# Performance work log

Hardware: AMD Instinct MI355X
Metric: run time of the kernel (lower is better)

## Reference

```python
import jax, jax.numpy as jnp
import numpy as np

N_HEAD = 16    # config.n_head
T_STEPS = 3    # config.T: PC energy-minimization steps
LR = 0.01      # config.local_learning_rate


def _causal_attention(x, Wq, Wk, Wv):
    # x: [B, S, E] latent activity; generative model f(x) = causal MHA(x)
    B, S, E = x.shape
    D = E // N_HEAD
    def split(h):  # [B,S,E] -> [B,H,S,D]
        return h.reshape(B, S, N_HEAD, D).transpose(0, 2, 1, 3)
    q = split(x @ Wq.T)
    k = split(x @ Wk.T)
    v = split(x @ Wv.T)
    scores = jnp.einsum('bhqd,bhkd->bhqk', q, k) / jnp.sqrt(jnp.asarray(D, x.dtype))
    mask = jnp.tril(jnp.ones((S, S), dtype=bool))
    scores = jnp.where(mask, scores, jnp.asarray(-1e30, x.dtype))
    att = jax.nn.softmax(scores, axis=-1)
    out = jnp.einsum('bhqk,bhkd->bhqd', att, v)
    return out.transpose(0, 2, 1, 3).reshape(B, S, E)


def _pc_infer(target, f):
    # PCLayer: T steps of gradient descent on E(x) = 0.5 * ||target - f(x)||^2
    # x_init = 'zeros'; returns the inferred latent x (PCLayer.get_x).
    x = jnp.zeros_like(target)
    energy = lambda z: 0.5 * jnp.sum((target - f(z)) ** 2)
    g = jax.grad(energy)
    for _ in range(T_STEPS):  # fixed small T: unrolled
        x = x - LR * g(x)
    return x


def setup_inputs() -> dict:
    key = jax.random.key(0)
    ks = jax.random.split(key, 5)
    B, S, E = 2, 1024, 1024
    fc1_x = jax.random.normal(ks[0], (B, S, E), dtype=jnp.float32)
    init = lambda k: 0.02 * jax.random.normal(k, (E, E), dtype=jnp.float32)
    return {
        'fc1_x': fc1_x,
        'Wq': init(ks[1]),
        'Wk': init(ks[2]),
        'Wv': init(ks[3]),
        'Wo': init(ks[4]),
    }


def reference(fc1_x, Wq, Wk, Wv, Wo):
    # Stage 1 (pc_output): infer pre-output latent att_score s.t. output-proj
    # Wo @ att_score ~ fc1_x  (generative model f1(x) = x @ Wo^T, bias=False).
    att_score = _pc_infer(fc1_x, lambda z: z @ Wo.T)
    # Stage 2 (pc_qkv): infer latent x_qkv s.t. causal MHA(x_qkv) ~ att_score.
    x_qkv = _pc_infer(att_score, lambda z: _causal_attention(z, Wq, Wk, Wv))
    return x_qkv
```

## Files before the change

kernel.cpp:

```cpp
#include <hip/hip_runtime.h>
#include <hip/hip_bf16.h>
#include <math.h>

#define S_LEN 1024
#define E_DIM 1024
#define NH 16
#define HD 64
#define M_ROWS 2048
#define BH_CNT 32

static constexpr float LR_C = 0.01f;
static constexpr float SC_C = 0.125f;
static constexpr float C2_C = 0.125f * 1.44269504f;

typedef unsigned short ushort_t;
typedef __attribute__((ext_vector_type(8))) __bf16 bf16x8;
typedef __attribute__((ext_vector_type(4))) float f32x4;

static __device__ inline ushort_t f2bu(float f) {
  __hip_bfloat16 h = __float2bfloat16(f);
  return *(ushort_t*)&h;
}
static __device__ inline bf16x8 ldg8(const ushort_t* p) { return *(const bf16x8*)p; }

static __device__ inline void async_cp16(const ushort_t* g, __bf16* lds_wave_base) {
  __builtin_amdgcn_global_load_lds((const __attribute__((address_space(1))) void*)g,
                                   (__attribute__((address_space(3))) void*)lds_wave_base,
                                   16, 0, 0);
}

static __device__ inline void stage_tile(const ushort_t* src, size_t src_stride,
                                         ushort_t* lds, int lane, int wave) {
  int rl = lane >> 3;
  int c = ((lane & 7) - rl) & 7;
  #pragma unroll
  for (int t = 0; t < 2; t++) {
    int s = wave * 2 + t;
    async_cp16(src + (size_t)(s * 8 + rl) * src_stride + c * 8,
               (__bf16*)(lds + s * 512));
  }
}
static __device__ inline const bf16x8* tile_at(const ushort_t* lds, int r, int cchunk) {
  return (const bf16x8*)(lds + r * 64 + (((cchunk + r) & 7) * 8));
}

__global__ __launch_bounds__(256) void prep_w(const float* __restrict__ W,
                                              ushort_t* __restrict__ Wb,
                                              ushort_t* __restrict__ WTb) {
  __shared__ float ts[64][65];
  int bx = blockIdx.x * 64, by = blockIdx.y * 64;
  int t = threadIdx.x;
  int rr = t >> 6, cc = t & 63;
  #pragma unroll
  for (int p = 0; p < 16; p++) {
    int r = p * 4 + rr;
    float v = W[(size_t)(by + r) * E_DIM + bx + cc];
    ts[r][cc] = v;
    Wb[(size_t)(by + r) * E_DIM + bx + cc] = f2bu(v);
  }
  __syncthreads();
  #pragma unroll
  for (int p = 0; p < 16; p++) {
    int r = p * 4 + rr;
    WTb[(size_t)(bx + r) * E_DIM + by + cc] = f2bu(ts[cc][r]);
  }
}

__global__ __launch_bounds__(256) void k_cast(const float* __restrict__ in,
                                              ushort_t* __restrict__ out, int n4) {
  int i = blockIdx.x * 256 + threadIdx.x;
  if (i < n4) {
    float4 v = ((const float4*)in)[i];
    ushort_t p[4] = {f2bu(v.x), f2bu(v.y), f2bu(v.z), f2bu(v.w)};
    *(uint2*)(out + (size_t)i * 4) = *(uint2*)p;
  }
}

__global__ __launch_bounds__(256) void k_formN(const float* __restrict__ Mf,
                                               const float* __restrict__ M2f,
                                               ushort_t* __restrict__ Nb) {
  int idx = blockIdx.x * 256 + threadIdx.x;
  int i = idx >> 10, j = idx & 1023;
  float v = -3.f * LR_C * LR_C * Mf[idx] + LR_C * LR_C * LR_C * M2f[idx];
  if (i == j) v += 3.f * LR_C;
  Nb[idx] = f2bu(v);
}

__global__ __launch_bounds__(256) void k_scan1(const float* __restrict__ Xs,
                                               float* __restrict__ Sf,
                                               float* __restrict__ tot) {
  int e = blockIdx.x * 256 + threadIdx.x;
  int b = blockIdx.y;
  int z = blockIdx.z;
  float acc = 0.f;
  for (int i = z * 64 + 63; i >= z * 64; i--) {
    size_t idx = ((size_t)b * S_LEN + i) * E_DIM + e;
    acc = fmaf(Xs[idx], 1.0f / (float)(i + 1), acc);
    Sf[idx] = acc;
  }
  tot[((size_t)b * 16 + z) * E_DIM + e] = acc;
}

__global__ __launch_bounds__(256) void k_scan2(const float* __restrict__ Sf,
                                               const float* __restrict__ tot,
                                               ushort_t* __restrict__ Sb) {
  int e = blockIdx.x * 256 + threadIdx.x;
  int b = blockIdx.y;
  int z = blockIdx.z;
  float off = 0.f;
  for (int c = z + 1; c < 16; c++) off += tot[((size_t)b * 16 + c) * E_DIM + e];
  for (int i = z * 64; i < z * 64 + 64; i++) {
    size_t idx = ((size_t)b * S_LEN + i) * E_DIM + e;
    Sb[idx] = f2bu(Sf[idx] + off);
  }
}

template <int MODE, int NSEG>
__global__ __launch_bounds__(256) void gemm_mf(
    const ushort_t* __restrict__ A0, const ushort_t* __restrict__ A1, const ushort_t* __restrict__ A2,
    const ushort_t* __restrict__ B0, const ushort_t* __restrict__ B1, const ushort_t* __restrict__ B2,
    float* __restrict__ Cf,
    ushort_t* __restrict__ Cb0,
    float alpha) {
  const int K = 1024;
  __shared__ __bf16 As0[64][32];
  __shared__ __bf16 As1[64][32];
  __shared__ __bf16 Bs0[64][32];
  __shared__ __bf16 Bs1[64][32];
  int tid = threadIdx.x;
  int m0 = blockIdx.y * 64, n0 = blockIdx.x * 64;

  int lane = tid & 63, wave = tid >> 6;
  int wrow = wave >> 1, wcol = wave & 1;
  int fr = lane & 15, q = lane >> 4;

  int srow = wave * 16 + (lane >> 2);
  int scg = ((lane & 3) + (srow >> 1)) & 3;
  int scol = scg * 8;
  __bf16* ldsA0 = &As0[wave * 16][0];
  __bf16* ldsA1 = &As1[wave * 16][0];
  __bf16* ldsB0 = &Bs0[wave * 16][0];
  __bf16* ldsB1 = &Bs1[wave * 16][0];

  int rA0 = wrow * 32 + fr, rA1r = rA0 + 16;
  int rB0 = wcol * 32 + fr, rB1r = rB0 + 16;
  int cA0 = ((q - (rA0 >> 1)) & 3) * 8;
  int cA1 = ((q - (rA1r >> 1)) & 3) * 8;
  int cB0 = ((q - (rB0 >> 1)) & 3) * 8;
  int cB1 = ((q - (rB1r >> 1)) & 3) * 8;
  const bf16x8* pa0h0 = (const bf16x8*)&As0[rA0][cA0];
  const bf16x8* pa0h1 = (const bf16x8*)&As1[rA0][cA0];
  const bf16x8* pa1h0 = (const bf16x8*)&As0[rA1r][cA1];
  const bf16x8* pa1h1 = (const bf16x8*)&As1[rA1r][cA1];
  const bf16x8* pb0h0 = (const bf16x8*)&Bs0[rB0][cB0];
  const bf16x8* pb0h1 = (const bf16x8*)&Bs1[rB0][cB0];
  const bf16x8* pb1h0 = (const bf16x8*)&Bs0[rB1r][cB1];
  const bf16x8* pb1h1 = (const bf16x8*)&Bs1[rB1r][cB1];

  f32x4 acc[2][2] = {};

  #pragma unroll 1
  for (int seg = 0; seg < NSEG; seg++) {
    const ushort_t* Aseg = (seg == 0) ? A0 : (seg == 1) ? A1 : A2;
    const ushort_t* Bseg = (seg == 0) ? B0 : (seg == 1) ? B1 : B2;
    const ushort_t* ga = Aseg + (size_t)(m0 + srow) * K + scol;
    const ushort_t* gb = Bseg + (size_t)(n0 + srow) * K + scol;
    #pragma unroll 1
    for (int k0 = 0; k0 < K; k0 += 64) {
      __syncthreads();
      async_cp16(ga + k0, ldsA0);
      async_cp16(ga + k0 + 32, ldsA1);
      async_cp16(gb + k0, ldsB0);
      async_cp16(gb + k0 + 32, ldsB1);
      __syncthreads();
      bf16x8 a00 = *pa0h0, a01 = *pa0h1, a10 = *pa1h0, a11 = *pa1h1;
      bf16x8 b00 = *pb0h0, b01 = *pb0h1, b10 = *pb1h0, b11 = *pb1h1;
      acc[0][0] = __builtin_amdgcn_mfma_f32_16x16x32_bf16(a00, b00, acc[0][0], 0, 0, 0);
      acc[0][1] = __builtin_amdgcn_mfma_f32_16x16x32_bf16(a00, b10, acc[0][1], 0, 0, 0);
      acc[1][0] = __builtin_amdgcn_mfma_f32_16x16x32_bf16(a10, b00, acc[1][0], 0, 0, 0);
      acc[1][1] = __builtin_amdgcn_mfma_f32_16x16x32_bf16(a10, b10, acc[1][1], 0, 0, 0);
      acc[0][0] = __builtin_amdgcn_mfma_f32_16x16x32_bf16(a01, b01, acc[0][0], 0, 0, 0);
      acc[0][1] = __builtin_amdgcn_mfma_f32_16x16x32_bf16(a01, b11, acc[0][1], 0, 0, 0);
      acc[1][0] = __builtin_amdgcn_mfma_f32_16x16x32_bf16(a11, b01, acc[1][0], 0, 0, 0);
      acc[1][1] = __builtin_amdgcn_mfma_f32_16x16x32_bf16(a11, b11, acc[1][1], 0, 0, 0);
    }
  }

  #pragma unroll
  for (int mi = 0; mi < 2; mi++)
    #pragma unroll
    for (int ni = 0; ni < 2; ni++) {
      int col = n0 + wcol * 32 + ni * 16 + fr;
      int row0 = m0 + wrow * 32 + mi * 16 + q * 4;
      #pragma unroll
      for (int r = 0; r < 4; r++) {
        size_t idx = (size_t)(row0 + r) * E_DIM + col;
        float v = acc[mi][ni][r];
        if (MODE == 3) {
          Cf[idx] = v;
        } else if (MODE == 4) {
          Cf[idx] = v;
          Cb0[idx] = f2bu(v);
        } else if (MODE == 6) {
          float nv = alpha * v;
          Cf[idx] = nv;
          Cb0[idx] = f2bu(nv);
        } else {
          Cb0[idx] = f2bu(v);
        }
      }
    }
}

__global__ __launch_bounds__(256) void gemm_qkv(
    const ushort_t* __restrict__ A,
    const ushort_t* __restrict__ B0, const ushort_t* __restrict__ B1, const ushort_t* __restrict__ B2,
    ushort_t* __restrict__ Cb0, ushort_t* __restrict__ Cb1, ushort_t* __restrict__ Cb2,
    ushort_t* __restrict__ Ct0, ushort_t* __restrict__ Ct1, ushort_t* __restrict__ Ct2) {
  const int K = 1024;
  __shared__ __bf16 As[2][64][32];
  __shared__ __bf16 Bs[3][2][64][32];
  int tid = threadIdx.x;
  int m0 = blockIdx.y * 64, n0 = blockIdx.x * 64;

  int lane = tid & 63, wave = tid >> 6;
  int wrow = wave >> 1, wcol = wave & 1;
  int fr = lane & 15, q = lane >> 4;

  int srow = wave * 16 + (lane >> 2);
  int scg = ((lane & 3) + (srow >> 1)) & 3;
  int scol = scg * 8;
  __bf16* ldsA0 = &As[0][wave * 16][0];
  __bf16* ldsA1 = &As[1][wave * 16][0];
  __bf16* ldsB00 = &Bs[0][0][wave * 16][0];
  __bf16* ldsB01 = &Bs[0][1][wave * 16][0];
  __bf16* ldsB10 = &Bs[1][0][wave * 16][0];
  __bf16* ldsB11 = &Bs[1][1][wave * 16][0];
  __bf16* ldsB20 = &Bs[2][0][wave * 16][0];
  __bf16* ldsB21 = &Bs[2][1][wave * 16][0];

  int rA0 = wrow * 32 + fr, rA1r = rA0 + 16;
  int rB0 = wcol * 32 + fr, rB1r = rB0 + 16;
  int cA0 = ((q - (rA0 >> 1)) & 3) * 8;
  int cA1 = ((q - (rA1r >> 1)) & 3) * 8;
  int cB0 = ((q - (rB0 >> 1)) & 3) * 8;
  int cB1 = ((q - (rB1r >> 1)) & 3) * 8;
  const bf16x8* pa0h0 = (const bf16x8*)&As[0][rA0][cA0];
  const bf16x8* pa0h1 = (const bf16x8*)&As[1][rA0][cA0];
  const bf16x8* pa1h0 = (const bf16x8*)&As[0][rA1r][cA1];
  const bf16x8* pa1h1 = (const bf16x8*)&As[1][rA1r][cA1];

  f32x4 acc[3][2][2] = {};

  const ushort_t* ga = A + (size_t)(m0 + srow) * K + scol;
  const ushort_t* gb0 = B0 + (size_t)(n0 + srow) * K + scol;
  const ushort_t* gb1 = B1 + (size_t)(n0 + srow) * K + scol;
  const ushort_t* gb2 = B2 + (size_t)(n0 + srow) * K + scol;

  #pragma unroll 1
  for (int k0 = 0; k0 < K; k0 += 64) {
    __syncthreads();
    async_cp16(ga + k0, ldsA0);
    async_cp16(ga + k0 + 32, ldsA1);
    async_cp16(gb0 + k0, ldsB00);
    async_cp16(gb0 + k0 + 32, ldsB01);
    async_cp16(gb1 + k0, ldsB10);
    async_cp16(gb1 + k0 + 32, ldsB11);
    async_cp16(gb2 + k0, ldsB20);
    async_cp16(gb2 + k0 + 32, ldsB21);
    __syncthreads();
    bf16x8 a00 = *pa0h0, a01 = *pa0h1, a10 = *pa1h0, a11 = *pa1h1;
    #pragma unroll
    for (int z = 0; z < 3; z++) {
      bf16x8 b00 = *(const bf16x8*)&Bs[z][0][rB0][cB0];
      bf16x8 b01 = *(const bf16x8*)&Bs[z][1][rB0][cB0];
      bf16x8 b10 = *(const bf16x8*)&Bs[z][0][rB1r][cB1];
      bf16x8 b11 = *(const bf16x8*)&Bs[z][1][rB1r][cB1];
      acc[z][0][0] = __builtin_amdgcn_mfma_f32_16x16x32_bf16(a00, b00, acc[z][0][0], 0, 0, 0);
      acc[z][0][1] = __builtin_amdgcn_mfma_f32_16x16x32_bf16(a00, b10, acc[z][0][1], 0, 0, 0);
      acc[z][1][0] = __builtin_amdgcn_mfma_f32_16x16x32_bf16(a10, b00, acc[z][1][0], 0, 0, 0);
      acc[z][1][1] = __builtin_amdgcn_mfma_f32_16x16x32_bf16(a10, b10, acc[z][1][1], 0, 0, 0);
      acc[z][0][0] = __builtin_amdgcn_mfma_f32_16x16x32_bf16(a01, b01, acc[z][0][0], 0, 0, 0);
      acc[z][0][1] = __builtin_amdgcn_mfma_f32_16x16x32_bf16(a01, b11, acc[z][0][1], 0, 0, 0);
      acc[z][1][0] = __builtin_amdgcn_mfma_f32_16x16x32_bf16(a11, b01, acc[z][1][0], 0, 0, 0);
      acc[z][1][1] = __builtin_amdgcn_mfma_f32_16x16x32_bf16(a11, b11, acc[z][1][1], 0, 0, 0);
    }
  }

  #pragma unroll
  for (int z = 0; z < 3; z++) {
    ushort_t* Cbz = (z == 0) ? Cb0 : (z == 1) ? Cb1 : Cb2;
    ushort_t* Ctz = (z == 0) ? Ct0 : (z == 1) ? Ct1 : Ct2;
    float tsc = (z == 2) ? 1.0f : SC_C;
    #pragma unroll
    for (int mi = 0; mi < 2; mi++)
      #pragma unroll
      for (int ni = 0; ni < 2; ni++) {
        int col = n0 + wcol * 32 + ni * 16 + fr;
        int row0 = m0 + wrow * 32 + mi * 16 + q * 4;
        ushort_t pk[4];
        #pragma unroll
        for (int r = 0; r < 4; r++) {
          size_t idx = (size_t)(row0 + r) * E_DIM + col;
          float v = acc[z][mi][ni][r];
          Cbz[idx] = f2bu(v);
          pk[r] = f2bu(v * tsc);
        }
        int hh = col >> 6, dd = col & 63;
        int bb = row0 >> 10, ss = row0 & 1023;
        *(uint2*)(Ctz + ((size_t)((bb * NH + hh) * HD + dd)) * S_LEN + ss) = *(uint2*)pk;
      }
  }
}

__global__ __launch_bounds__(256) void gemm_acc(
    const ushort_t* __restrict__ A0, const ushort_t* __restrict__ A1, const ushort_t* __restrict__ A2,
    const ushort_t* __restrict__ B0, const ushort_t* __restrict__ B1, const ushort_t* __restrict__ B2,
    float* __restrict__ Cf, ushort_t* __restrict__ Cb, float alpha) {
  const int K = 1024;
  __shared__ __bf16 As[3][2][64][32];
  __shared__ __bf16 Bs[3][2][64][32];
  int tid = threadIdx.x;
  int m0 = blockIdx.y * 64, n0 = blockIdx.x * 64;

  int lane = tid & 63, wave = tid >> 6;
  int wrow = wave >> 1, wcol = wave & 1;
  int fr = lane & 15, q = lane >> 4;

  int srow = wave * 16 + (lane >> 2);
  int scg = ((lane & 3) + (srow >> 1)) & 3;
  int scol = scg * 8;

  int rA0 = wrow * 32 + fr, rA1r = rA0 + 16;
  int rB0 = wcol * 32 + fr, rB1r = rB0 + 16;
  int cA0 = ((q - (rA0 >> 1)) & 3) * 8;
  int cA1 = ((q - (rA1r >> 1)) & 3) * 8;
  int cB0 = ((q - (rB0 >> 1)) & 3) * 8;
  int cB1 = ((q - (rB1r >> 1)) & 3) * 8;

  f32x4 acc[3][2][2] = {};

  const ushort_t* ga0 = A0 + (size_t)(m0 + srow) * K + scol;
  const ushort_t* ga1 = A1 + (size_t)(m0 + srow) * K + scol;
  const ushort_t* ga2 = A2 + (size_t)(m0 + srow) * K + scol;
  const ushort_t* gb0 = B0 + (size_t)(n0 + srow) * K + scol;
  const ushort_t* gb1 = B1 + (size_t)(n0 + srow) * K + scol;
  const ushort_t* gb2 = B2 + (size_t)(n0 + srow) * K + scol;

  #pragma unroll 1
  for (int k0 = 0; k0 < K; k0 += 64) {
    __syncthreads();
    async_cp16(ga0 + k0,      &As[0][0][wave * 16][0]);
    async_cp16(ga0 + k0 + 32, &As[0][1][wave * 16][0]);
    async_cp16(ga1 + k0,      &As[1][0][wave * 16][0]);
    async_cp16(ga1 + k0 + 32, &As[1][1][wave * 16][0]);
    async_cp16(ga2 + k0,      &As[2][0][wave * 16][0]);
    async_cp16(ga2 + k0 + 32, &As[2][1][wave * 16][0]);
    async_cp16(gb0 + k0,      &Bs[0][0][wave * 16][0]);
    async_cp16(gb0 + k0 + 32, &Bs[0][1][wave * 16][0]);
    async_cp16(gb1 + k0,      &Bs[1][0][wave * 16][0]);
    async_cp16(gb1 + k0 + 32, &Bs[1][1][wave * 16][0]);
    async_cp16(gb2 + k0,      &Bs[2][0][wave * 16][0]);
    async_cp16(gb2 + k0 + 32, &Bs[2][1][wave * 16][0]);
    __syncthreads();
    #pragma unroll
    for (int z = 0; z < 3; z++) {
      bf16x8 a00 = *(const bf16x8*)&As[z][0][rA0][cA0];
      bf16x8 a01 = *(const bf16x8*)&As[z][1][rA0][cA0];
      bf16x8 a10 = *(const bf16x8*)&As[z][0][rA1r][cA1];
      bf16x8 a11 = *(const bf16x8*)&As[z][1][rA1r][cA1];
      bf16x8 b00 = *(const bf16x8*)&Bs[z][0][rB0][cB0];
      bf16x8 b01 = *(const bf16x8*)&Bs[z][1][rB0][cB0];
      bf16x8 b10 = *(const bf16x8*)&Bs[z][0][rB1r][cB1];
      bf16x8 b11 = *(const bf16x8*)&Bs[z][1][rB1r][cB1];
      acc[z][0][0] = __builtin_amdgcn_mfma_f32_16x16x32_bf16(a00, b00, acc[z][0][0], 0, 0, 0);
      acc[z][0][1] = __builtin_amdgcn_mfma_f32_16x16x32_bf16(a00, b10, acc[z][0][1], 0, 0, 0);
      acc[z][1][0] = __builtin_amdgcn_mfma_f32_16x16x32_bf16(a10, b00, acc[z][1][0], 0, 0, 0);
      acc[z][1][1] = __builtin_amdgcn_mfma_f32_16x16x32_bf16(a10, b10, acc[z][1][1], 0, 0, 0);
      acc[z][0][0] = __builtin_amdgcn_mfma_f32_16x16x32_bf16(a01, b01, acc[z][0][0], 0, 0, 0);
      acc[z][0][1] = __builtin_amdgcn_mfma_f32_16x16x32_bf16(a01, b11, acc[z][0][1], 0, 0, 0);
      acc[z][1][0] = __builtin_amdgcn_mfma_f32_16x16x32_bf16(a11, b01, acc[z][1][0], 0, 0, 0);
      acc[z][1][1] = __builtin_amdgcn_mfma_f32_16x16x32_bf16(a11, b11, acc[z][1][1], 0, 0, 0);
    }
  }

  #pragma unroll
  for (int mi = 0; mi < 2; mi++)
    #pragma unroll
    for (int ni = 0; ni < 2; ni++) {
      int col = n0 + wcol * 32 + ni * 16 + fr;
      int row0 = m0 + wrow * 32 + mi * 16 + q * 4;
      #pragma unroll
      for (int r = 0; r < 4; r++) {
        size_t idx = (size_t)(row0 + r) * E_DIM + col;
        float v = (acc[0][mi][ni][r] + acc[1][mi][ni][r]) + acc[2][mi][ni][r];
        float nv = Cf[idx] + alpha * v;
        Cf[idx] = nv;
        Cb[idx] = f2bu(nv);
      }
    }
}


__global__ __launch_bounds__(256) void fwd_fused(const ushort_t* __restrict__ Qg,
                                                 const ushort_t* __restrict__ Kg,
                                                 const ushort_t* __restrict__ Vt,
                                                 const float* __restrict__ Xs,
                                                 float* __restrict__ mbuf,
                                                 ushort_t* __restrict__ Gb,
                                                 ushort_t* __restrict__ Gt,
                                                 float* __restrict__ Dv) {
  int bh = blockIdx.x, y = blockIdx.y;
  int it = (y < 8) ? (15 - y) : (y - 8);
  int b = bh >> 4, h = bh & 15;
  int tid = threadIdx.x, lane = tid & 63, wv = tid >> 6;
  int fr = lane & 15, q = lane >> 4;
  int i0 = it * 64, band = wv * 16;
  __shared__ ushort_t Ksb[2][4096];
  __shared__ ushort_t Vsb[2][4096];
  __shared__ ushort_t Ps[64][72];

  const ushort_t* Kbase = Kg + (size_t)(b * S_LEN) * E_DIM + h * HD;
  const ushort_t* Vbase = Vt + (size_t)(bh * HD) * S_LEN;

  const ushort_t* Qrow = Qg + (size_t)(b * S_LEN + i0 + band + fr) * E_DIM + h * HD;
  bf16x8 aq0 = ldg8(Qrow + q * 8);
  bf16x8 aq1 = ldg8(Qrow + 32 + q * 8);

  float m[4], l[4];
  #pragma unroll
  for (int r = 0; r < 4; r++) { m[r] = -1e30f; l[r] = 0.f; }
  f32x4 oacc[4] = {};

  stage_tile(Kbase, E_DIM, Ksb[0], lane, wv);
  stage_tile(Vbase, S_LEN, Vsb[0], lane, wv);

  #pragma unroll 1
  for (int jt = 0; jt <= it; jt++) {
    int j0 = jt * 64;
    int cur = jt & 1;
    __syncthreads();
    if (jt < it) {
      int j0n = j0 + 64;
      stage_tile(Kbase + (size_t)j0n * E_DIM, E_DIM, Ksb[cur ^ 1], lane, wv);
      stage_tile(Vbase + j0n, S_LEN, Vsb[cur ^ 1], lane, wv);
    }
    const ushort_t* Ks = Ksb[cur];
    const ushort_t* Vs = Vsb[cur];
    f32x4 sA[4];
    #pragma unroll
    for (int nc = 0; nc < 4; nc++) {
      bf16x8 bk0 = *tile_at(Ks, nc * 16 + fr, q);
      bf16x8 bk1 = *tile_at(Ks, nc * 16 + fr, q + 4);
      f32x4 z = {};
      z = __builtin_amdgcn_mfma_f32_16x16x32_bf16(aq0, bk0, z, 0, 0, 0);
      sA[nc] = __builtin_amdgcn_mfma_f32_16x16x32_bf16(aq1, bk1, z, 0, 0, 0);
    }
    float sv[4][4];
    if (jt == it) {
      #pragma unroll
      for (int nc = 0; nc < 4; nc++)
        #pragma unroll
        for (int r = 0; r < 4; r++) {
          int row = i0 + band + q * 4 + r;
          int col = j0 + nc * 16 + fr;
          sv[nc][r] = (col <= row) ? sA[nc][r] * C2_C : -1e30f;
        }
    } else {
      #pragma unroll
      for (int nc = 0; nc < 4; nc++)
        #pragma unroll
        for (int r = 0; r < 4; r++)
          sv[nc][r] = sA[nc][r] * C2_C;
    }
    #pragma unroll
    for (int r = 0; r < 4; r++) {
      float mx = fmaxf(fmaxf(sv[0][r], sv[1][r]), fmaxf(sv[2][r], sv[3][r]));
      #pragma unroll
      for (int off = 1; off < 16; off <<= 1) mx = fmaxf(mx, __shfl_xor(mx, off, 64));
      float mn = fmaxf(m[r], mx);
      float alpha = exp2f(m[r] - mn);
      float ps = 0.f;
      #pragma unroll
      for (int nc = 0; nc < 4; nc++) {
        float p = exp2f(sv[nc][r] - mn);
        Ps[band + q * 4 + r][nc * 16 + fr] = f2bu(p);
        ps += p;
      }
      l[r] = l[r] * alpha + ps;
      m[r] = mn;
      #pragma unroll
      for (int nc = 0; nc < 4; nc++) oacc[nc][r] *= alpha;
    }
    bf16x8 ap0 = *(const bf16x8*)&Ps[band + fr][q * 8];
    bf16x8 ap1 = *(const bf16x8*)&Ps[band + fr][32 + q * 8];
    #pragma unroll
    for (int nc = 0; nc < 4; nc++) {
      bf16x8 bv0 = *tile_at(Vs, nc * 16 + fr, q);
      bf16x8 bv1 = *tile_at(Vs, nc * 16 + fr, q + 4);
      oacc[nc] = __builtin_amdgcn_mfma_f32_16x16x32_bf16(ap0, bv0, oacc[nc], 0, 0, 0);
      oacc[nc] = __builtin_amdgcn_mfma_f32_16x16x32_bf16(ap1, bv1, oacc[nc], 0, 0, 0);
    }
  }
  #pragma unroll
  for (int r = 0; r < 4; r++) {
    #pragma unroll
    for (int off = 1; off < 16; off <<= 1) l[r] += __shfl_xor(l[r], off, 64);
  }
  float linv[4];
  #pragma unroll
  for (int r = 0; r < 4; r++) linv[r] = 1.0f / l[r];
  float dpart[4] = {};
  #pragma unroll
  for (int nc = 0; nc < 4; nc++) {
    ushort_t pg[4];
    #pragma unroll
    for (int r = 0; r < 4; r++) {
      int row = i0 + band + q * 4 + r;
      size_t gi = (size_t)(b * S_LEN + row) * E_DIM + h * HD + nc * 16 + fr;
      float o = oacc[nc][r] * linv[r];
      float g = o - Xs[gi];
      ushort_t bu = f2bu(g);
      Gb[gi] = bu;
      pg[r] = bu;
      dpart[r] += g * o;
    }
    int d = nc * 16 + fr;
    int s0 = i0 + band + q * 4;
    *(uint2*)(Gt + ((size_t)bh * HD + d) * S_LEN + s0) = *(uint2*)pg;
  }
  #pragma unroll
  for (int r = 0; r < 4; r++) {
    #pragma unroll
    for (int off = 1; off < 16; off <<= 1) dpart[r] += __shfl_xor(dpart[r], off, 64);
  }
  if (fr == 0) {
    #pragma unroll
    for (int r = 0; r < 4; r++) {
      size_t sid = (size_t)bh * S_LEN + i0 + band + q * 4 + r;
      mbuf[sid] = m[r] + log2f(l[r]);
      Dv[sid] = dpart[r];
    }
  }
}

__global__ __launch_bounds__(256) void bwd_fused(const ushort_t* __restrict__ Qg,
                                                 const ushort_t* __restrict__ Kg,
                                                 const ushort_t* __restrict__ Vg,
                                                 const ushort_t* __restrict__ Gg,
                                                 const ushort_t* __restrict__ Qt,
                                                 const ushort_t* __restrict__ Kt,
                                                 const ushort_t* __restrict__ Gt,
                                                 const float* __restrict__ mbuf,
                                                 const float* __restrict__ Dv,
                                                 ushort_t* __restrict__ GQ,
                                                 ushort_t* __restrict__ GK,
                                                 ushort_t* __restrict__ GV) {
  int bh = blockIdx.x, y = blockIdx.y;
  int b = bh >> 4, h = bh & 15;
  int tid = threadIdx.x, lane = tid & 63, wv = tid >> 6;
  int fr = lane & 15, q = lane >> 4;
  int band = wv * 16;
  __shared__ ushort_t tA[4][4096];
  __shared__ ushort_t tP[2][64][72];

  {
    ushort_t* Ks = tA[0];
    ushort_t* Vs = tA[1];
    ushort_t* Ts = tA[2];
    ushort_t (*dSs)[72] = tP[0];
    int it = y, i0 = it * 64;

    const ushort_t* KbaseA = Kg + (size_t)(b * S_LEN) * E_DIM + h * HD;
    const ushort_t* VbaseA = Vg + (size_t)(b * S_LEN) * E_DIM + h * HD;
    const ushort_t* TbaseA = Kt + (size_t)(bh * HD) * S_LEN;

    const ushort_t* Qrow = Qg + (size_t)(b * S_LEN + i0 + band + fr) * E_DIM + h * HD;
    const ushort_t* Grow = Gg + (size_t)(b * S_LEN + i0 + band + fr) * E_DIM + h * HD;
    bf16x8 aq0 = ldg8(Qrow + q * 8), aq1 = ldg8(Qrow + 32 + q * 8);
    bf16x8 ag0 = ldg8(Grow + q * 8), ag1 = ldg8(Grow + 32 + q * 8);

    float mrow[4], Dr[4];
    #pragma unroll
    for (int r = 0; r < 4; r++) {
      size_t sid = (size_t)bh * S_LEN + i0 + band + q * 4 + r;
      mrow[r] = mbuf[sid]; Dr[r] = Dv[sid];
    }
    f32x4 dqacc[4] = {};

    #pragma unroll 1
    for (int jt = 0; jt <= it; jt++) {
      int j0 = jt * 64;
      __syncthreads();
      stage_tile(KbaseA + (size_t)j0 * E_DIM, E_DIM, Ks, lane, wv);
      stage_tile(VbaseA + (size_t)j0 * E_DIM, E_DIM, Vs, lane, wv);
      stage_tile(TbaseA + j0, S_LEN, Ts, lane, wv);
      __syncthreads();
      f32x4 sA[4], dpA[4];
      #pragma unroll
      for (int nc = 0; nc < 4; nc++) {
        bf16x8 bk0 = *tile_at(Ks, nc * 16 + fr, q);
        bf16x8 bk1 = *tile_at(Ks, nc * 16 + fr, q + 4);
        bf16x8 bv0 = *tile_at(Vs, nc * 16 + fr, q);
        bf16x8 bv1 = *tile_at(Vs, nc * 16 + fr, q + 4);
        f32x4 z = {};
        z = __builtin_amdgcn_mfma_f32_16x16x32_bf16(aq0, bk0, z, 0, 0, 0);
        sA[nc] = __builtin_amdgcn_mfma_f32_16x16x32_bf16(aq1, bk1, z, 0, 0, 0);
        f32x4 z2 = {};
        z2 = __builtin_amdgcn_mfma_f32_16x16x32_bf16(ag0, bv0, z2, 0, 0, 0);
        dpA[nc] = __builtin_amdgcn_mfma_f32_16x16x32_bf16(ag1, bv1, z2, 0, 0, 0);
      }
      if (jt == it) {
        #pragma unroll
        for (int nc = 0; nc < 4; nc++)
          #pragma unroll
          for (int r = 0; r < 4; r++) {
            int row = i0 + band + q * 4 + r;
            int col = j0 + nc * 16 + fr;
            float ds = 0.f;
            if (col <= row) {
              float P = exp2f(fmaf(sA[nc][r], C2_C, -mrow[r]));
              ds = P * (dpA[nc][r] - Dr[r]);
            }
            dSs[band + q * 4 + r][nc * 16 + fr] = f2bu(ds);
          }
      } else {
        #pragma unroll
        for (int nc = 0; nc < 4; nc++)
          #pragma unroll
          for (int r = 0; r < 4; r++) {
            float P = exp2f(fmaf(sA[nc][r], C2_C, -mrow[r]));
            float ds = P * (dpA[nc][r] - Dr[r]);
            dSs[band + q * 4 + r][nc * 16 + fr] = f2bu(ds);
          }
      }
      bf16x8 ad0 = *(const bf16x8*)&dSs[band + fr][q * 8];
      bf16x8 ad1 = *(const bf16x8*)&dSs[band + fr][32 + q * 8];
      #pragma unroll
      for (int nc = 0; nc < 4; nc++) {
        bf16x8 bt0 = *tile_at(Ts, nc * 16 + fr, q);
        bf16x8 bt1 = *tile_at(Ts, nc * 16 + fr, q + 4);
        dqacc[nc] = __builtin_amdgcn_mfma_f32_16x16x32_bf16(ad0, bt0, dqacc[nc], 0, 0, 0);
        dqacc[nc] = __builtin_amdgcn_mfma_f32_16x16x32_bf16(ad1, bt1, dqacc[nc], 0, 0, 0);
      }
    }
    #pragma unroll
    for (int nc = 0; nc < 4; nc++)
      #pragma unroll
      for (int r = 0; r < 4; r++) {
        int row = i0 + band + q * 4 + r;
        size_t gi = (size_t)(b * S_LEN + row) * E_DIM + h * HD + nc * 16 + fr;
        GQ[gi] = f2bu(dqacc[nc][r]);
      }
  }

  {
    ushort_t* Qs  = tA[0];
    ushort_t* Gs  = tA[1];
    ushort_t* Qts = tA[2];
    ushort_t* Gts = tA[3];
    ushort_t (*PT)[72]  = tP[0];
    ushort_t (*dST)[72] = tP[1];
    int jt = y, j0 = jt * 64;

    const ushort_t* QbaseB = Qg + (size_t)(b * S_LEN) * E_DIM + h * HD;
    const ushort_t* GbaseB = Gg + (size_t)(b * S_LEN) * E_DIM + h * HD;
    const ushort_t* QtbaseB = Qt + (size_t)(bh * HD) * S_LEN;
    const ushort_t* GtbaseB = Gt + (size_t)(bh * HD) * S_LEN;

    const ushort_t* Krow = Kg + (size_t)(b * S_LEN + j0 + band + fr) * E_DIM + h * HD;
    const ushort_t* Vrow = Vg + (size_t)(b * S_LEN + j0 + band + fr) * E_DIM + h * HD;
    bf16x8 ak0 = ldg8(Krow + q * 8), ak1 = ldg8(Krow + 32 + q * 8);
    bf16x8 av0 = ldg8(Vrow + q * 8), av1 = ldg8(Vrow + 32 + q * 8);

    f32x4 dkacc[4] = {}, dvacc[4] = {};

    #pragma unroll 1
    for (int i_t = jt; i_t < 16; i_t++) {
      int i0 = i_t * 64;
      __syncthreads();
      stage_tile(QbaseB + (size_t)i0 * E_DIM, E_DIM, Qs, lane, wv);
      stage_tile(GbaseB + (size_t)i0 * E_DIM, E_DIM, Gs, lane, wv);
      stage_tile(QtbaseB + i0, S_LEN, Qts, lane, wv);
      stage_tile(GtbaseB + i0, S_LEN, Gts, lane, wv);
      __syncthreads();
      float mc[4], Dc[4];
      #pragma unroll
      for (int nc = 0; nc < 4; nc++) {
        size_t sid = (size_t)bh * S_LEN + i0 + nc * 16 + fr;
        mc[nc] = mbuf[sid]; Dc[nc] = Dv[sid];
      }
      f32x4 stA[4], dptA[4];
      #pragma unroll
      for (int nc = 0; nc < 4; nc++) {
        bf16x8 bq0 = *tile_at(Qs, nc * 16 + fr, q);
        bf16x8 bq1 = *tile_at(Qs, nc * 16 + fr, q + 4);
        bf16x8 bg0 = *tile_at(Gs, nc * 16 + fr, q);
        bf16x8 bg1 = *tile_at(Gs, nc * 16 + fr, q + 4);
        f32x4 z = {};
        z = __builtin_amdgcn_mfma_f32_16x16x32_bf16(ak0, bq0, z, 0, 0, 0);
        stA[nc] = __builtin_amdgcn_mfma_f32_16x16x32_bf16(ak1, bq1, z, 0, 0, 0);
        f32x4 z2 = {};
        z2 = __builtin_amdgcn_mfma_f32_16x16x32_bf16(av0, bg0, z2, 0, 0, 0);
        dptA[nc] = __builtin_amdgcn_mfma_f32_16x16x32_bf16(av1, bg1, z2, 0, 0, 0);
      }
      if (i_t == jt) {
        #pragma unroll
        for (int nc = 0; nc < 4; nc++)
          #pragma unroll
          for (int r = 0; r < 4; r++) {
            int jrow = j0 + band + q * 4 + r;
            int icol = i0 + nc * 16 + fr;
            float P = 0.f, ds = 0.f;
            if (icol >= jrow) {
              P = exp2f(fmaf(stA[nc][r], C2_C, -mc[nc]));
              ds = P * (dptA[nc][r] - Dc[nc]);
            }
            PT[band + q * 4 + r][nc * 16 + fr] = f2bu(P);
            dST[band + q * 4 + r][nc * 16 + fr] = f2bu(ds);
          }
      } else {
        #pragma unroll
        for (int nc = 0; nc < 4; nc++)
          #pragma unroll
          for (int r = 0; r < 4; r++) {
            float P = exp2f(fmaf(stA[nc][r], C2_C, -mc[nc]));
            float ds = P * (dptA[nc][r] - Dc[nc]);
            PT[band + q * 4 + r][nc * 16 + fr] = f2bu(P);
            dST[band + q * 4 + r][nc * 16 + fr] = f2bu(ds);
          }
      }
      bf16x8 ap0 = *(const bf16x8*)&PT[band + fr][q * 8];
      bf16x8 ap1 = *(const bf16x8*)&PT[band + fr][32 + q * 8];
      bf16x8 ad0 = *(const bf16x8*)&dST[band + fr][q * 8];
      bf16x8 ad1 = *(const bf16x8*)&dST[band + fr][32 + q * 8];
      #pragma unroll
      for (int nc = 0; nc < 4; nc++) {
        bf16x8 bg0 = *tile_at(Gts, nc * 16 + fr, q);
        bf16x8 bg1 = *tile_at(Gts, nc * 16 + fr, q + 4);
        bf16x8 bq0 = *tile_at(Qts, nc * 16 + fr, q);
        bf16x8 bq1 = *tile_at(Qts, nc * 16 + fr, q + 4);
        dvacc[nc] = __builtin_amdgcn_mfma_f32_16x16x32_bf16(ap0, bg0, dvacc[nc], 0, 0, 0);
        dvacc[nc] = __builtin_amdgcn_mfma_f32_16x16x32_bf16(ap1, bg1, dvacc[nc], 0, 0, 0);
        dkacc[nc] = __builtin_amdgcn_mfma_f32_16x16x32_bf16(ad0, bq0, dkacc[nc], 0, 0, 0);
        dkacc[nc] = __builtin_amdgcn_mfma_f32_16x16x32_bf16(ad1, bq1, dkacc[nc], 0, 0, 0);
      }
    }
    #pragma unroll
    for (int nc = 0; nc < 4; nc++)
      #pragma unroll
      for (int r = 0; r < 4; r++) {
        int jrow = j0 + band + q * 4 + r;
        size_t gi = (size_t)(b * S_LEN + jrow) * E_DIM + h * HD + nc * 16 + fr;
        GK[gi] = f2bu(dkacc[nc][r]);
        GV[gi] = f2bu(dvacc[nc][r]);
      }
  }
}

extern "C" void kernel_launch(void* const* d_in, const int* in_sizes, int n_in,
                              void* d_out, int out_size, void* d_ws, size_t ws_size,
                              hipStream_t stream) {
  const float* T1 = (const float*)d_in[0];
  const float* Wq = (const float*)d_in[1];
  const float* Wk = (const float*)d_in[2];
  const float* Wv = (const float*)d_in[3];
  const float* Wo = (const float*)d_in[4];

  const size_t M2 = 2097152;
  const size_t M1 = 1048576;
  float* w = (float*)d_ws;
  float* Xs = w;
  float* mS = Xs + M2;
  float* DvS = mS + 65536;
  ushort_t* u = (ushort_t*)(DvS + 65536);
  ushort_t* W0 = u;          ushort_t* W1 = W0 + M1;  ushort_t* W2 = W1 + M1;
  ushort_t* W3 = W2 + M1;    ushort_t* W4 = W3 + M1;  ushort_t* W5 = W4 + M1;
  ushort_t* Qb = W5 + M1;    ushort_t* Kb = Qb + M2;  ushort_t* Vb = Kb + M2;
  ushort_t* Qt = Vb + M2;    ushort_t* Kt = Qt + M2;  ushort_t* Vt = Kt + M2;
  ushort_t* Gt = Vt + M2;
  ushort_t* Gb = Gt + M2;
  ushort_t* GQb = Gb + M2;   ushort_t* GKb = GQb + M2; ushort_t* GVb = GKb + M2;
  ushort_t* X2b = GVb + M2;
  float* X2 = (float*)d_out;

  float* Mf  = (float*)Qb;
  float* M2f = (float*)Kb;
  ushort_t* Mb  = Gt;
  ushort_t* Nb  = Vb;
  ushort_t* AtB = Qt;
  ushort_t* T1b = Kt;

  float* Sf  = (float*)GQb;
  float* tot = mS;
  ushort_t* Sb = GVb;

  dim3 pgrid(16, 16);
  dim3 sgrid(16, 16);
  dim3 ggrid(16, 32);
  dim3 agrid(BH_CNT, 16);

  k_cast<<<(M2 / 4 + 255) / 256, 256, 0, stream>>>(T1, T1b, (int)(M2 / 4));
  prep_w<<<pgrid, 256, 0, stream>>>(Wo, W0, W1);
  gemm_mf<4, 1><<<sgrid, 256, 0, stream>>>(W1, nullptr, nullptr, W1, nullptr, nullptr,
                                           Mf, Mb, 0.f);
  gemm_mf<3, 1><<<sgrid, 256, 0, stream>>>(Mb, nullptr, nullptr, Mb, nullptr, nullptr,
                                           M2f, nullptr, 0.f);
  k_formN<<<(M1 + 255) / 256, 256, 0, stream>>>(Mf, M2f, Nb);
  gemm_mf<5, 1><<<sgrid, 256, 0, stream>>>(Nb, nullptr, nullptr, W0, nullptr, nullptr,
                                           nullptr, AtB, 0.f);
  prep_w<<<pgrid, 256, 0, stream>>>(Wq, W0, W3);
  prep_w<<<pgrid, 256, 0, stream>>>(Wk, W1, W4);
  prep_w<<<pgrid, 256, 0, stream>>>(Wv, W2, W5);
  gemm_mf<3, 1><<<ggrid, 256, 0, stream>>>(T1b, nullptr, nullptr, AtB, nullptr, nullptr,
                                           Xs, nullptr, 0.f);

  k_scan1<<<dim3(E_DIM / 256, 2, 16), 256, 0, stream>>>(Xs, Sf, tot);
  k_scan2<<<dim3(E_DIM / 256, 2, 16), 256, 0, stream>>>(Sf, tot, Sb);
  gemm_mf<6, 1><<<ggrid, 256, 0, stream>>>(Sb, nullptr, nullptr, W5, nullptr, nullptr,
                                           X2, X2b, LR_C);

  for (int t = 1; t < 3; t++) {
    gemm_qkv<<<ggrid, 256, 0, stream>>>(X2b, W0, W1, W2,
                                        Qb, Kb, Vb, Qt, Kt, Vt);
    fwd_fused<<<agrid, 256, 0, stream>>>(Qb, Kb, Vt, Xs, mS, Gb, Gt, DvS);
    bwd_fused<<<agrid, 256, 0, stream>>>(Qb, Kb, Vb, Gb, Qt, Kt, Gt, mS, DvS,
                                         GQb, GKb, GVb);
    gemm_acc<<<ggrid, 256, 0, stream>>>(GQb, GKb, GVb, W3, W4, W5,
                                        X2, X2b, -LR_C);
  }
}
```

Baseline: 407.7 us.

## Double-buffer GEMM LDS tiles, merge weight prep, fuse formN into GEMM epilogue

Adds double-buffered LDS staging to gemm_mf and gemm_qkv so the async copies for the next K-tile are issued while MFMAs consume the current one, dropping one barrier per iteration. The four weight-prep launches become one launch with a z grid dimension. The N-matrix formation kernel is folded into a new epilogue mode of the M^2 GEMM, which removes a kernel and an fp32 intermediate. Shared memory per block doubles, which may reduce occupancy. The per-iteration barrier now sits before the prefetch issue, so correctness depends on how async_cp16 completion is waited on.

```diff
diff --git a/kernel.cpp b/kernel.cpp
--- a/kernel.cpp
+++ b/kernel.cpp
@@ -44,10 +44,18 @@
   return (const bf16x8*)(lds + r * 64 + (((cchunk + r) & 7) * 8));
 }
 
-__global__ __launch_bounds__(256) void prep_w(const float* __restrict__ W,
-                                              ushort_t* __restrict__ Wb,
-                                              ushort_t* __restrict__ WTb) {
+__global__ __launch_bounds__(256) void prep_w4(
+    const float* __restrict__ Wo, const float* __restrict__ Wq,
+    const float* __restrict__ Wk, const float* __restrict__ Wv,
+    ushort_t* __restrict__ o0, ushort_t* __restrict__ t0,
+    ushort_t* __restrict__ o1, ushort_t* __restrict__ t1,
+    ushort_t* __restrict__ o2, ushort_t* __restrict__ t2,
+    ushort_t* __restrict__ o3, ushort_t* __restrict__ t3) {
   __shared__ float ts[64][65];
+  int z = blockIdx.z;
+  const float* W = (z == 0) ? Wo : (z == 1) ? Wq : (z == 2) ? Wk : Wv;
+  ushort_t* Wb  = (z == 0) ? o0 : (z == 1) ? o1 : (z == 2) ? o2 : o3;
+  ushort_t* WTb = (z == 0) ? t0 : (z == 1) ? t1 : (z == 2) ? t2 : t3;
   int bx = blockIdx.x * 64, by = blockIdx.y * 64;
   int t = threadIdx.x;
   int rr = t >> 6, cc = t & 63;
@@ -74,16 +82,6 @@
     ushort_t p[4] = {f2bu(v.x), f2bu(v.y), f2bu(v.z), f2bu(v.w)};
     *(uint2*)(out + (size_t)i * 4) = *(uint2*)p;
   }
-}
-
-__global__ __launch_bounds__(256) void k_formN(const float* __restrict__ Mf,
-                                               const float* __restrict__ M2f,
-                                               ushort_t* __restrict__ Nb) {
-  int idx = blockIdx.x * 256 + threadIdx.x;
-  int i = idx >> 10, j = idx & 1023;
-  float v = -3.f * LR_C * LR_C * Mf[idx] + LR_C * LR_C * LR_C * M2f[idx];
-  if (i == j) v += 3.f * LR_C;
-  Nb[idx] = f2bu(v);
 }
 
 __global__ __launch_bounds__(256) void k_scan1(const float* __restrict__ Xs,
@@ -115,18 +113,13 @@
   }
 }
 
-template <int MODE, int NSEG>
+template <int MODE>
 __global__ __launch_bounds__(256) void gemm_mf(
-    const ushort_t* __restrict__ A0, const ushort_t* __restrict__ A1, const ushort_t* __restrict__ A2,
-    const ushort_t* __restrict__ B0, const ushort_t* __restrict__ B1, const ushort_t* __restrict__ B2,
-    float* __restrict__ Cf,
-    ushort_t* __restrict__ Cb0,
-    float alpha) {
+    const ushort_t* __restrict__ A, const ushort_t* __restrict__ B,
+    float* __restrict__ Cf, ushort_t* __restrict__ Cb0, float alpha) {
   const int K = 1024;
-  __shared__ __bf16 As0[64][32];
-  __shared__ __bf16 As1[64][32];
-  __shared__ __bf16 Bs0[64][32];
-  __shared__ __bf16 Bs1[64][32];
+  __shared__ __bf16 As[2][2][64][32];
+  __shared__ __bf16 Bs[2][2][64][32];
   int tid = threadIdx.x;
   int m0 = blockIdx.y * 64, n0 = blockIdx.x * 64;
 
@@ -137,10 +130,6 @@
   int srow = wave * 16 + (lane >> 2);
   int scg = ((lane & 3) + (srow >> 1)) & 3;
   int scol = scg * 8;
-  __bf16* ldsA0 = &As0[wave * 16][0];
-  __bf16* ldsA1 = &As1[wave * 16][0];
-  __bf16* ldsB0 = &Bs0[wave * 16][0];
-  __bf16* ldsB1 = &Bs1[wave * 16][0];
 
   int rA0 = wrow * 32 + fr, rA1r = rA0 + 16;
   int rB0 = wcol * 32 + fr, rB1r = rB0 + 16;
@@ -148,42 +137,44 @@
   int cA1 = ((q - (rA1r >> 1)) & 3) * 8;
   int cB0 = ((q - (rB0 >> 1)) & 3) * 8;
   int cB1 = ((q - (rB1r >> 1)) & 3) * 8;
-  const bf16x8* pa0h0 = (const bf16x8*)&As0[rA0][cA0];
-  const bf16x8* pa0h1 = (const bf16x8*)&As1[rA0][cA0];
-  const bf16x8* pa1h0 = (const bf16x8*)&As0[rA1r][cA1];
-  const bf16x8* pa1h1 = (const bf16x8*)&As1[rA1r][cA1];
-  const bf16x8* pb0h0 = (const bf16x8*)&Bs0[rB0][cB0];
-  const bf16x8* pb0h1 = (const bf16x8*)&Bs1[rB0][cB0];
-  const bf16x8* pb1h0 = (const bf16x8*)&Bs0[rB1r][cB1];
-  const bf16x8* pb1h1 = (const bf16x8*)&Bs1[rB1r][cB1];
+
+  const ushort_t* ga = A + (size_t)(m0 + srow) * K + scol;
+  const ushort_t* gb = B + (size_t)(n0 + srow) * K + scol;
 
   f32x4 acc[2][2] = {};
 
+  async_cp16(ga,      &As[0][0][wave * 16][0]);
+  async_cp16(ga + 32, &As[0][1][wave * 16][0]);
+  async_cp16(gb,      &Bs[0][0][wave * 16][0]);
+  async_cp16(gb + 32, &Bs[0][1][wave * 16][0]);
+
   #pragma unroll 1
-  for (int seg = 0; seg < NSEG; seg++) {
-    const ushort_t* Aseg = (seg == 0) ? A0 : (seg == 1) ? A1 : A2;
-    const ushort_t* Bseg = (seg == 0) ? B0 : (seg == 1) ? B1 : B2;
-    const ushort_t* ga = Aseg + (size_t)(m0 + srow) * K + scol;
-    const ushort_t* gb = Bseg + (size_t)(n0 + srow) * K + scol;
-    #pragma unroll 1
-    for (int k0 = 0; k0 < K; k0 += 64) {
-      __syncthreads();
-      async_cp16(ga + k0, ldsA0);
-      async_cp16(ga + k0 + 32, ldsA1);
-      async_cp16(gb + k0, ldsB0);
-      async_cp16(gb + k0 + 32, ldsB1);
-      __syncthreads();
-      bf16x8 a00 = *pa0h0, a01 = *pa0h1, a10 = *pa1h0, a11 = *pa1h1;
-      bf16x8 b00 = *pb0h0, b01 = *pb0h1, b10 = *pb1h0, b11 = *pb1h1;
-      acc[0][0] = __builtin_amdgcn_mfma_f32_16x16x32_bf16(a00, b00, acc[0][0], 0, 0, 0);
-      acc[0][1] = __builtin_amdgcn_mfma_f32_16x16x32_bf16(a00, b10, acc[0][1], 0, 0, 0);
-      acc[1][0] = __builtin_amdgcn_mfma_f32_16x16x32_bf16(a10, b00, acc[1][0], 0, 0, 0);
-      acc[1][1] = __builtin_amdgcn_mfma_f32_16x16x32_bf16(a10, b10, acc[1][1], 0, 0, 0);
-      acc[0][0] = __builtin_amdgcn_mfma_f32_16x16x32_bf16(a01, b01, acc[0][0], 0, 0, 0);
-      acc[0][1] = __builtin_amdgcn_mfma_f32_16x16x32_bf16(a01, b11, acc[0][1], 0, 0, 0);
-      acc[1][0] = __builtin_amdgcn_mfma_f32_16x16x32_bf16(a11, b01, acc[1][0], 0, 0, 0);
-      acc[1][1] = __builtin_amdgcn_mfma_f32_16x16x32_bf16(a11, b11, acc[1][1], 0, 0, 0);
-    }
+  for (int k0 = 0; k0 < K; k0 += 64) {
+    int cur = (k0 >> 6) & 1;
+    __syncthreads();
+    if (k0 + 64 < K) {
+      int nxt = cur ^ 1;
+      async_cp16(ga + k0 + 64, &As[nxt][0][wave * 16][0]);
+      async_cp16(ga + k0 + 96, &As[nxt][1][wave * 16][0]);
+      async_cp16(gb + k0 + 64, &Bs[nxt][0][wave * 16][0]);
+      async_cp16(gb + k0 + 96, &Bs[nxt][1][wave * 16][0]);
+    }
+    bf16x8 a00 = *(const bf16x8*)&As[cur][0][rA0][cA0];
+    bf16x8 a01 = *(const bf16x8*)&As[cur][1][rA0][cA0];
+    bf16x8 a10 = *(const bf16x8*)&As[cur][0][rA1r][cA1];
+    bf16x8 a11 = *(const bf16x8*)&As[cur][1][rA1r][cA1];
+    bf16x8 b00 = *(const bf16x8*)&Bs[cur][0][rB0][cB0];
+    bf16x8 b01 = *(const bf16x8*)&Bs[cur][1][rB0][cB0];
+    bf16x8 b10 = *(const bf16x8*)&Bs[cur][0][rB1r][cB1];
+    bf16x8 b11 = *(const bf16x8*)&Bs[cur][1][rB1r][cB1];
+    acc[0][0] = __builtin_amdgcn_mfma_f32_16x16x32_bf16(a00, b00, acc[0][0], 0, 0, 0);
+    acc[0][1] = __builtin_amdgcn_mfma_f32_16x16x32_bf16(a00, b10, acc[0][1], 0, 0, 0);
+    acc[1][0] = __builtin_amdgcn_mfma_f32_16x16x32_bf16(a10, b00, acc[1][0], 0, 0, 0);
+    acc[1][1] = __builtin_amdgcn_mfma_f32_16x16x32_bf16(a10, b10, acc[1][1], 0, 0, 0);
+    acc[0][0] = __builtin_amdgcn_mfma_f32_16x16x32_bf16(a01, b01, acc[0][0], 0, 0, 0);
+    acc[0][1] = __builtin_amdgcn_mfma_f32_16x16x32_bf16(a01, b11, acc[0][1], 0, 0, 0);
+    acc[1][0] = __builtin_amdgcn_mfma_f32_16x16x32_bf16(a11, b01, acc[1][0], 0, 0, 0);
+    acc[1][1] = __builtin_amdgcn_mfma_f32_16x16x32_bf16(a11, b11, acc[1][1], 0, 0, 0);
   }
 
   #pragma unroll
@@ -205,6 +196,10 @@
           float nv = alpha * v;
           Cf[idx] = nv;
           Cb0[idx] = f2bu(nv);
+        } else if (MODE == 7) {
+          float nv = -3.f * LR_C * LR_C * Cf[idx] + LR_C * LR_C * LR_C * v;
+          if (row0 + r == col) nv += 3.f * LR_C;
+          Cb0[idx] = f2bu(nv);
         } else {
           Cb0[idx] = f2bu(v);
         }
@@ -218,8 +213,8 @@
     ushort_t* __restrict__ Cb0, ushort_t* __restrict__ Cb1, ushort_t* __restrict__ Cb2,
     ushort_t* __restrict__ Ct0, ushort_t* __restrict__ Ct1, ushort_t* __restrict__ Ct2) {
   const int K = 1024;
-  __shared__ __bf16 As[2][64][32];
-  __shared__ __bf16 Bs[3][2][64][32];
+  __shared__ __bf16 As[2][2][64][32];
+  __shared__ __bf16 Bs[2][3][2][64][32];
   int tid = threadIdx.x;
   int m0 = blockIdx.y * 64, n0 = blockIdx.x * 64;
 
@@ -230,14 +225,6 @@
   int srow = wave * 16 + (lane >> 2);
   int scg = ((lane & 3) + (srow >> 1)) & 3;
   int scol = scg * 8;
-  __bf16* ldsA0 = &As[0][wave * 16][0];
-  __bf16* ldsA1 = &As[1][wave * 16][0];
-  __bf16* ldsB00 = &Bs[0][0][wave * 16][0];
-  __bf16* ldsB01 = &Bs[0][1][wave * 16][0];
-  __bf16* ldsB10 = &Bs[1][0][wave * 16][0];
-  __bf16* ldsB11 = &Bs[1][1][wave * 16][0];
-  __bf16* ldsB20 = &Bs[2][0][wave * 16][0];
-  __bf16* ldsB21 = &Bs[2][1][wave * 16][0];
 
   int rA0 = wrow * 32 + fr, rA1r = rA0 + 16;
   int rB0 = wcol * 32 + fr, rB1r = rB0 + 16;
@@ -245,37 +232,48 @@
   int cA1 = ((q - (rA1r >> 1)) & 3) * 8;
   int cB0 = ((q - (rB0 >> 1)) & 3) * 8;
   int cB1 = ((q - (rB1r >> 1)) & 3) * 8;
-  const bf16x8* pa0h0 = (const bf16x8*)&As[0][rA0][cA0];
-  const bf16x8* pa0h1 = (const bf16x8*)&As[1][rA0][cA0];
-  const bf16x8* pa1h0 = (const bf16x8*)&As[0][rA1r][cA1];
-  const bf16x8* pa1h1 = (const bf16x8*)&As[1][rA1r][cA1];
-
-  f32x4 acc[3][2][2] = {};
 
   const ushort_t* ga = A + (size_t)(m0 + srow) * K + scol;
   const ushort_t* gb0 = B0 + (size_t)(n0 + srow) * K + scol;
   const ushort_t* gb1 = B1 + (size_t)(n0 + srow) * K + scol;
   const ushort_t* gb2 = B2 + (size_t)(n0 + srow) * K + scol;
 
+  f32x4 acc[3][2][2] = {};
+
+  async_cp16(ga,       &As[0][0][wave * 16][0]);
+  async_cp16(ga + 32,  &As[0][1][wave * 16][0]);
+  async_cp16(gb0,      &Bs[0][0][0][wave * 16][0]);
+  async_cp16(gb0 + 32, &Bs[0][0][1][wave * 16][0]);
+  async_cp16(gb1,      &Bs[0][1][0][wave * 16][0]);
+  async_cp16(gb1 + 32, &Bs[0][1][1][wave * 16][0]);
+  async_cp16(gb2,      &Bs[0][2][0][wave * 16][0]);
+  async_cp16(gb2 + 32, &Bs[0][2][1][wave * 16][0]);
+
   #pragma unroll 1
   for (int k0 = 0; k0 < K; k0 += 64) {
+    int cur = (k0 >> 6) & 1;
     __syncthreads();
-    async_cp16(ga + k0, ldsA0);
-    async_cp16(ga + k0 + 32, ldsA1);
-    async_cp16(gb0 + k0, ldsB00);
-    async_cp16(gb0 + k0 + 32, ldsB01);
-    async_cp16(gb1 + k0, ldsB10);
-    async_cp16(gb1 + k0 + 32, ldsB11);
-    async_cp16(gb2 + k0, ldsB20);
-    async_cp16(gb2 + k0 + 32, ldsB21);
-    __syncthreads();
-    bf16x8 a00 = *pa0h0, a01 = *pa0h1, a10 = *pa1h0, a11 = *pa1h1;
+    if (k0 + 64 < K) {
+      int nxt = cur ^ 1;
+      async_cp16(ga + k0 + 64,  &As[nxt][0][wave * 16][0]);
+      async_cp16(ga + k0 + 96,  &As[nxt][1][wave * 16][0]);
+      async_cp16(gb0 + k0 + 64, &Bs[nxt][0][0][wave * 16][0]);
+      async_cp16(gb0 + k0 + 96, &Bs[nxt][0][1][wave * 16][0]);
+      async_cp16(gb1 + k0 + 64, &Bs[nxt][1][0][wave * 16][0]);
+      async_cp16(gb1 + k0 + 96, &Bs[nxt][1][1][wave * 16][0]);
+      async_cp16(gb2 + k0 + 64, &Bs[nxt][2][0][wave * 16][0]);
+      async_cp16(gb2 + k0 + 96, &Bs[nxt][2][1][wave * 16][0]);
+    }
+    bf16x8 a00 = *(const bf16x8*)&As[cur][0][rA0][cA0];
+    bf16x8 a01 = *(const bf16x8*)&As[cur][1][rA0][cA0];
+    bf16x8 a10 = *(const bf16x8*)&As[cur][0][rA1r][cA1];
+    bf16x8 a11 = *(const bf16x8*)&As[cur][1][rA1r][cA1];
     #pragma unroll
     for (int z = 0; z < 3; z++) {
-      bf16x8 b00 = *(const bf16x8*)&Bs[z][0][rB0][cB0];
-      bf16x8 b01 = *(const bf16x8*)&Bs[z][1][rB0][cB0];
-      bf16x8 b10 = *(const bf16x8*)&Bs[z][0][rB1r][cB1];
-      bf16x8 b11 = *(const bf16x8*)&Bs[z][1][rB1r][cB1];
+      bf16x8 b00 = *(const bf16x8*)&Bs[cur][z][0][rB0][cB0];
+      bf16x8 b01 = *(const bf16x8*)&Bs[cur][z][1][rB0][cB0];
+      bf16x8 b10 = *(const bf16x8*)&Bs[cur][z][0][rB1r][cB1];
+      bf16x8 b11 = *(const bf16x8*)&Bs[cur][z][1][rB1r][cB1];
       acc[z][0][0] = __builtin_amdgcn_mfma_f32_16x16x32_bf16(a00, b00, acc[z][0][0], 0, 0, 0);
       acc[z][0][1] = __builtin_amdgcn_mfma_f32_16x16x32_bf16(a00, b10, acc[z][0][1], 0, 0, 0);
       acc[z][1][0] = __builtin_amdgcn_mfma_f32_16x16x32_bf16(a10, b00, acc[z][1][0], 0, 0, 0);
@@ -784,9 +782,10 @@
   ushort_t* X2b = GVb + M2;
   float* X2 = (float*)d_out;
 
+  ushort_t* WoB = Gb;
+  ushort_t* WoT = Gt;
   float* Mf  = (float*)Qb;
-  float* M2f = (float*)Kb;
-  ushort_t* Mb  = Gt;
+  ushort_t* Mb  = Vt;
   ushort_t* Nb  = Vb;
   ushort_t* AtB = Qt;
   ushort_t* T1b = Kt;
@@ -795,30 +794,22 @@
   float* tot = mS;
   ushort_t* Sb = GVb;
 
-  dim3 pgrid(16, 16);
+  dim3 p4grid(16, 16, 4);
   dim3 sgrid(16, 16);
   dim3 ggrid(16, 32);
   dim3 agrid(BH_CNT, 16);
 
+  prep_w4<<<p4grid, 256, 0, stream>>>(Wo, Wq, Wk, Wv,
+                                      WoB, WoT, W0, W3, W1, W4, W2, W5);
   k_cast<<<(M2 / 4 + 255) / 256, 256, 0, stream>>>(T1, T1b, (int)(M2 / 4));
-  prep_w<<<pgrid, 256, 0, stream>>>(Wo, W0, W1);
-  gemm_mf<4, 1><<<sgrid, 256, 0, stream>>>(W1, nullptr, nullptr, W1, nullptr, nullptr,
-                                           Mf, Mb, 0.f);
-  gemm_mf<3, 1><<<sgrid, 256, 0, stream>>>(Mb, nullptr, nullptr, Mb, nullptr, nullptr,
-                                           M2f, nullptr, 0.f);
-  k_formN<<<(M1 + 255) / 256, 256, 0, stream>>>(Mf, M2f, Nb);
-  gemm_mf<5, 1><<<sgrid, 256, 0, stream>>>(Nb, nullptr, nullptr, W0, nullptr, nullptr,
-                                           nullptr, AtB, 0.f);
-  prep_w<<<pgrid, 256, 0, stream>>>(Wq, W0, W3);
-  prep_w<<<pgrid, 256, 0, stream>>>(Wk, W1, W4);
-  prep_w<<<pgrid, 256, 0, stream>>>(Wv, W2, W5);
-  gemm_mf<3, 1><<<ggrid, 256, 0, stream>>>(T1b, nullptr, nullptr, AtB, nullptr, nullptr,
-                                           Xs, nullptr, 0.f);
+  gemm_mf<4><<<sgrid, 256, 0, stream>>>(WoT, WoT, Mf, Mb, 0.f);
+  gemm_mf<7><<<sgrid, 256, 0, stream>>>(Mb, Mb, Mf, Nb, 0.f);
+  gemm_mf<5><<<sgrid, 256, 0, stream>>>(Nb, WoB, nullptr, AtB, 0.f);
+  gemm_mf<3><<<ggrid, 256, 0, stream>>>(T1b, AtB, Xs, nullptr, 0.f);
 
   k_scan1<<<dim3(E_DIM / 256, 2, 16), 256, 0, stream>>>(Xs, Sf, tot);
   k_scan2<<<dim3(E_DIM / 256, 2, 16), 256, 0, stream>>>(Sf, tot, Sb);
-  gemm_mf<6, 1><<<ggrid, 256, 0, stream>>>(Sb, nullptr, nullptr, W5, nullptr, nullptr,
-                                           X2, X2b, LR_C);
+  gemm_mf<6><<<ggrid, 256, 0, stream>>>(Sb, W5, X2, X2b, LR_C);
 
   for (int t = 1; t < 3; t++) {
     gemm_qkv<<<ggrid, 256, 0, stream>>>(X2b, W0, W1, W2,
```

Measured after the change: 389.6 us. 4.4% less time.
